# Kernel optimization log

Hardware: AMD Instinct MI355X
Metric: run time of the kernel (lower is better)

The kernel has to match this reference:

```python
import jax, jax.numpy as jnp
import numpy as np


def setup_inputs() -> dict:
    key = jax.random.key(0)
    ks = jax.random.split(key, 4)
    B, Tq, Tv = 8, 1024, 1024
    Dq, Dv, Do = 1024, 1024, 1024
    scale_q = 1.0 / np.sqrt(Dq)
    scale_2 = 1.0 / np.sqrt(Dq + Dv)
    return {
        "query": jax.random.normal(ks[0], (B, Tq, Dq), jnp.float32),
        "values": jax.random.normal(ks[1], (B, Tv, Dv), jnp.float32),
        "W1": jax.random.normal(ks[2], (Dv, Dq), jnp.float32) * scale_q,
        "b1": jnp.zeros((Dv,), jnp.float32),
        "W2": jax.random.normal(ks[3], (Do, Dq + Dv), jnp.float32) * scale_2,
        "b2": jnp.zeros((Do,), jnp.float32),
    }


def reference(query, values, W1, b1, W2, b2):
    # linear1: project query into values space  [B, Tq, Dv]
    q_resize = jnp.einsum("btd,vd->btv", query, W1) + b1
    # attention scores [B, Tq, Tv] and softmax over keys
    scores = jnp.einsum("bqd,bkd->bqk", q_resize, values)
    attn = jax.nn.softmax(scores, axis=-1)
    # attended values [B, Tq, Dv]
    attended = jnp.einsum("bqk,bkd->bqd", attn, values)
    # concat + linear2 + tanh
    feed = jnp.concatenate([attended, query], axis=-1)
    out = jnp.tanh(jnp.einsum("btf,of->bto", feed, W2) + b2)
    return out
```

## Files before the change

### kernel.cpp

```cpp
#include <hip/hip_runtime.h>
#include <hip/hip_bf16.h>

typedef __bf16 bf16x8 __attribute__((ext_vector_type(8)));
typedef float f32x4 __attribute__((ext_vector_type(4)));
typedef unsigned short u16;
typedef unsigned short us4 __attribute__((ext_vector_type(4)));
typedef unsigned int u32;

__device__ __forceinline__ u16 f2bf(float x) {
  union { float f; u32 u; } v; v.f = x;
  u32 r = v.u + 0x7FFFu + ((v.u >> 16) & 1u);
  return (u16)(r >> 16);
}
__device__ __forceinline__ float bf2f(u16 h) {
  union { u32 u; float f; } v; v.u = ((u32)h) << 16;
  return v.f;
}

__device__ __forceinline__ void glds16(const void* g, void* l) {
  __builtin_amdgcn_global_load_lds(
      (const __attribute__((address_space(1))) void*)g,
      (__attribute__((address_space(3))) void*)l, 16, 0, 0);
}

#define BARRIER_FENCED() do {                        \
  __builtin_amdgcn_sched_barrier(0);                 \
  __builtin_amdgcn_s_barrier();                      \
  __builtin_amdgcn_sched_barrier(0);                 \
} while (0)

template<int NSEG, int EPI>
__global__ __launch_bounds__(512, 2)
void gemm_bt(const u16* __restrict__ A, const u16* __restrict__ B,
             void* __restrict__ Cout, const float* __restrict__ bias,
             int K0, int lda, int ldb, int ldc,
             long sA, long sB, long sC, int nx, int ny)
{
  __shared__ __align__(1024) char lds_raw[3 * 49152];

  const int d = blockIdx.x;
  const int L = ((d & 7) << 5) | (d >> 3);
  const int nxy = nx * ny;
  const int bz = L / nxy;
  const int rr = L - bz * nxy;
  const int bx = rr / ny;
  const int by = rr - bx * ny;
  const int brow = bx * 256;
  const int bcol = by * 128;

  const int tid  = threadIdx.x;
  const int wid  = tid >> 6;
  const int lane = tid & 63;
  const int kh   = wid >> 2;
  const int wr   = (wid >> 1) & 1;
  const int wc   = wid & 1;

  const u16* Ab = A + (long)bz * sA + (long)brow * lda;
  const u16* Bb = B + (long)bz * sB + (long)bcol * ldb;

  f32x4 acc[8][4];
#pragma unroll
  for (int m = 0; m < 8; ++m)
#pragma unroll
    for (int n = 0; n < 4; ++n) acc[m][n] = (f32x4){0.f, 0.f, 0.f, 0.f};

  const int ksteps = (NSEG == 3) ? 16 : (K0 >> 6);
  const int NT = NSEG * ksteps;

  const int r15 = lane & 15;
  const int c16 = (lane >> 4) * 8;

  auto stage = [&](int t, int b) {
    int seg, kt;
    if (NSEG == 3) { seg = t >> 4; kt = (t & 15) << 6; }
    else           { seg = 0;      kt = t << 6; }
    const u16* Aseg = Ab + ((NSEG == 3 && seg == 1) ? K0 : 0) + kt;
    const u16* Bseg = Bb + ((NSEG == 3 && seg == 2) ? K0 : 0) + kt;
    u16* Lb = (u16*)(lds_raw + b * 49152);
#pragma unroll
    for (int q = 0; q < 4; ++q) {
      const int fa = wid * 4 + q;
      const int mi = fa >> 1, ki = fa & 1;
      glds16(Aseg + (long)(mi * 16 + r15) * lda + ki * 32 + c16, Lb + fa * 512);
    }
#pragma unroll
    for (int q = 0; q < 2; ++q) {
      const int fb = wid * 2 + q;
      const int nj = fb >> 1, ki = fb & 1;
      glds16(Bseg + (long)(nj * 16 + r15) * ldb + ki * 32 + c16,
             Lb + 16384 + fb * 512);
    }
  };

  stage(0, 0);
  stage(1, 1);
  asm volatile("s_waitcnt vmcnt(6)" ::: "memory");
  BARRIER_FENCED();

  int bufc = 0;
  for (int t = 0; t < NT; ++t) {
    const u16* Lb = (const u16*)(lds_raw + bufc * 49152);
    const u16* Af = Lb + (wr * 16 + kh) * 512 + lane * 8;
    const u16* Bf = Lb + 16384 + (wc * 8 + kh) * 512 + lane * 8;
    bf16x8 a[8], b[4];
#pragma unroll
    for (int m = 0; m < 8; ++m) a[m] = *(const bf16x8*)(Af + m * 1024);
#pragma unroll
    for (int n = 0; n < 4; ++n) b[n] = *(const bf16x8*)(Bf + n * 1024);

    if (t + 2 < NT) {
      int bufs = bufc + 2; if (bufs >= 3) bufs -= 3;
      stage(t + 2, bufs);
    }

    __builtin_amdgcn_s_setprio(1);
#pragma unroll
    for (int m = 0; m < 8; ++m)
#pragma unroll
      for (int n = 0; n < 4; ++n)
        acc[m][n] = __builtin_amdgcn_mfma_f32_16x16x32_bf16(a[m], b[n], acc[m][n], 0, 0, 0);
    __builtin_amdgcn_s_setprio(0);

    if (t + 2 < NT) { asm volatile("s_waitcnt vmcnt(6)" ::: "memory"); }
    else            { asm volatile("s_waitcnt vmcnt(0)" ::: "memory"); }
    BARRIER_FENCED();
    bufc = bufc + 1; if (bufc >= 3) bufc = 0;
  }

  float* red = (float*)lds_raw;
  const int p = wr * 2 + wc;
  if (kh == 1) {
#pragma unroll
    for (int m = 0; m < 8; ++m)
#pragma unroll
      for (int n = 0; n < 4; ++n)
        *(f32x4*)(red + ((p * 32 + m * 4 + n) * 64 + lane) * 4) = acc[m][n];
  }
  asm volatile("s_waitcnt lgkmcnt(0)" ::: "memory");
  BARRIER_FENCED();

  if (kh == 0) {
#pragma unroll
    for (int m = 0; m < 8; ++m)
#pragma unroll
      for (int n = 0; n < 4; ++n)
        acc[m][n] += *(const f32x4*)(red + ((p * 32 + m * 4 + n) * 64 + lane) * 4);

    const int crow0 = brow + wr * 128;
    const int ccol0 = bcol + wc * 64;
    const int orow  = (lane >> 4) * 4;
    const int ocol  = lane & 15;
#pragma unroll
    for (int m = 0; m < 8; ++m) {
#pragma unroll
      for (int n = 0; n < 4; ++n) {
        const int col = ccol0 + n * 16 + ocol;
        float bv = 0.f;
        if (EPI == 1 || EPI == 3) bv = bias[col];
#pragma unroll
        for (int j = 0; j < 4; ++j) {
          const int row = crow0 + m * 16 + orow + j;
          float v = acc[m][n][j] + bv;
          if (EPI == 0) {
            ((float*)Cout)[(long)bz * sC + (long)row * ldc + col] = v;
          } else if (EPI == 1) {
            u16 hi = f2bf(v);
            u16 lo = f2bf(v - bf2f(hi));
            u16* Co = (u16*)Cout + (long)bz * sC + (long)row * ldc;
            Co[col] = hi;
            Co[col + 1024] = lo;
          } else if (EPI == 2) {
            ((u16*)Cout)[(long)bz * sC + (long)row * ldc + col] = f2bf(v);
          } else {
            ((float*)Cout)[(long)bz * sC + (long)row * ldc + col] = tanhf(v);
          }
        }
      }
    }
  }
}

__global__ __launch_bounds__(256)
void split_pack(const float* __restrict__ X, u16* __restrict__ P,
                u16* __restrict__ FQ, long n4)
{
  long i = (long)blockIdx.x * 256 + threadIdx.x;
  const long stride = (long)gridDim.x * 256;
  for (; i < n4; i += stride) {
    float4 x = ((const float4*)X)[i];
    long e = i * 4;
    long row = e >> 10;
    int col = (int)(e & 1023);
    float xs[4] = {x.x, x.y, x.z, x.w};
    u16 h[4], l[4];
#pragma unroll
    for (int j = 0; j < 4; ++j) {
      h[j] = f2bf(xs[j]);
      l[j] = f2bf(xs[j] - bf2f(h[j]));
    }
    us4 hv = {h[0], h[1], h[2], h[3]};
    us4 lv = {l[0], l[1], l[2], l[3]};
    *(us4*)(P + row * 2048 + col) = hv;
    *(us4*)(P + row * 2048 + 1024 + col) = lv;
    if (FQ) *(us4*)(FQ + row * 2048 + 1024 + col) = hv;
  }
}

__global__ __launch_bounds__(256)
void conv_values(const float* __restrict__ V, u16* __restrict__ Vp,
                 u16* __restrict__ VT)
{
  __shared__ u16 tile[64][68];
  const int b  = blockIdx.z;
  const int d0 = blockIdx.x * 64;
  const int k0 = blockIdx.y * 64;
  const int t  = threadIdx.x;
  const int tr = t >> 4;
  const int tc = (t & 15) * 4;
  const float* Vb = V + (long)b * (1024L * 1024);
  u16* Vpb = Vp + (long)b * (1024L * 2048);
  u16* VTb = VT + (long)b * (1024L * 1024);

#pragma unroll
  for (int i = 0; i < 4; ++i) {
    int k = tr + i * 16;
    float4 x = *(const float4*)(Vb + (long)(k0 + k) * 1024 + d0 + tc);
    float xs[4] = {x.x, x.y, x.z, x.w};
    u16 h[4], l[4];
#pragma unroll
    for (int j = 0; j < 4; ++j) {
      h[j] = f2bf(xs[j]);
      l[j] = f2bf(xs[j] - bf2f(h[j]));
      tile[k][tc + j] = h[j];
    }
    us4 hv = {h[0], h[1], h[2], h[3]};
    us4 lv = {l[0], l[1], l[2], l[3]};
    *(us4*)(Vpb + (long)(k0 + k) * 2048 + d0 + tc) = hv;
    *(us4*)(Vpb + (long)(k0 + k) * 2048 + 1024 + d0 + tc) = lv;
  }
  __syncthreads();
#pragma unroll
  for (int i = 0; i < 4; ++i) {
    int d = tr + i * 16;
    int k = tc;
    us4 o = {tile[k][d], tile[k + 1][d], tile[k + 2][d], tile[k + 3][d]};
    *(us4*)(VTb + (long)(d0 + d) * 1024 + k0 + k) = o;
  }
}

__global__ __launch_bounds__(256)
void conv_cast(const float* __restrict__ X, u16* __restrict__ Y, long n4)
{
  long i = (long)blockIdx.x * 256 + threadIdx.x;
  const long stride = (long)gridDim.x * 256;
  for (; i < n4; i += stride) {
    float4 x = ((const float4*)X)[i];
    us4 o = {f2bf(x.x), f2bf(x.y), f2bf(x.z), f2bf(x.w)};
    *(us4*)(Y + i * 4) = o;
  }
}

__global__ __launch_bounds__(256)
void softmax_rows(const float* __restrict__ S, u16* __restrict__ A)
{
  const long row = blockIdx.x;
  const float* src = S + row * 1024;
  const int t = threadIdx.x;
  const int lane = t & 63, wid = t >> 6;
  float4 v = ((const float4*)src)[t];
  float m = fmaxf(fmaxf(v.x, v.y), fmaxf(v.z, v.w));
#pragma unroll
  for (int off = 32; off >= 1; off >>= 1)
    m = fmaxf(m, __shfl_xor(m, off));
  __shared__ float redm[4];
  if (lane == 0) redm[wid] = m;
  __syncthreads();
  m = fmaxf(fmaxf(redm[0], redm[1]), fmaxf(redm[2], redm[3]));
  float e0 = __expf(v.x - m), e1 = __expf(v.y - m);
  float e2 = __expf(v.z - m), e3 = __expf(v.w - m);
  float s = e0 + e1 + e2 + e3;
#pragma unroll
  for (int off = 32; off >= 1; off >>= 1)
    s += __shfl_xor(s, off);
  __shared__ float reds[4];
  if (lane == 0) reds[wid] = s;
  __syncthreads();
  s = reds[0] + reds[1] + reds[2] + reds[3];
  float inv = 1.0f / s;
  us4 o = {f2bf(e0 * inv), f2bf(e1 * inv), f2bf(e2 * inv), f2bf(e3 * inv)};
  ((us4*)(A + row * 1024))[t] = o;
}

extern "C" void kernel_launch(void* const* d_in, const int* in_sizes, int n_in,
                              void* d_out, int out_size, void* d_ws, size_t ws_size,
                              hipStream_t stream)
{
  const float* query  = (const float*)d_in[0];
  const float* values = (const float*)d_in[1];
  const float* W1     = (const float*)d_in[2];
  const float* b1     = (const float*)d_in[3];
  const float* W2     = (const float*)d_in[4];
  const float* b2     = (const float*)d_in[5];
  float* out = (float*)d_out;

  char* ws = (char*)d_ws;
  const long MB = 1024L * 1024;
  u16*   W1p    = (u16*)(ws);
  u16*   W2b    = (u16*)(ws + 4 * MB);
  u16*   Aq     = (u16*)(ws + 8 * MB);
  float* scores = (float*)(ws + 8 * MB);
  u16*   qr     = (u16*)(ws + 40 * MB);
  u16*   attn   = (u16*)(ws + 40 * MB);
  u16*   Vp     = (u16*)(ws + 72 * MB);
  u16*   VT     = (u16*)(ws + 104 * MB);
  u16*   feed   = (u16*)(ws + 120 * MB);

  split_pack<<<dim3(2048), dim3(256), 0, stream>>>(query, Aq, feed, (8192L * 1024) / 4);
  split_pack<<<dim3(1024), dim3(256), 0, stream>>>(W1, W1p, (u16*)nullptr, (1024L * 1024) / 4);
  conv_values<<<dim3(16, 16, 8), dim3(256), 0, stream>>>(values, Vp, VT);
  conv_cast<<<dim3(1024), dim3(256), 0, stream>>>(W2, W2b, (1024L * 2048) / 4);

  gemm_bt<3, 1><<<dim3(256), dim3(512), 0, stream>>>(
      Aq, W1p, qr, b1, 1024, 2048, 2048, 2048, 0L, 0L, 0L, 32, 8);

  gemm_bt<3, 0><<<dim3(256), dim3(512), 0, stream>>>(
      qr, Vp, scores, (const float*)nullptr, 1024, 2048, 2048, 1024,
      1024L * 2048, 1024L * 2048, 1024L * 1024, 4, 8);

  softmax_rows<<<dim3(8192), dim3(256), 0, stream>>>(scores, attn);

  gemm_bt<1, 2><<<dim3(256), dim3(512), 0, stream>>>(
      attn, VT, feed, (const float*)nullptr, 1024, 1024, 1024, 2048,
      1024L * 1024, 1024L * 1024, 1024L * 2048, 4, 8);

  gemm_bt<1, 3><<<dim3(256), dim3(512), 0, stream>>>(
      feed, W2b, out, b2, 2048, 2048, 2048, 1024, 0L, 0L, 0L, 32, 8);
}
```

Measured before the change: 395.2 us.

## Split GEMM k-step into four interleaved phases with barriers and staged loads

Breaks each k-step of the bf16 MFMA GEMM main loop into four phases. Each phase loads two A fragments from LDS, issues part of the next stage's global-to-LDS copies, and then runs eight MFMAs. Barriers and sched_barrier keep the waves in lockstep. The aim is to spread LDS reads and global loads across the MFMA work so they overlap better, in the style of ping-pong scheduling. The cost is many extra workgroup barriers per iteration, which can stall waves.

```diff
diff --git a/kernel.cpp b/kernel.cpp
--- a/kernel.cpp
+++ b/kernel.cpp
@@ -70,19 +70,22 @@
   const int r15 = lane & 15;
   const int c16 = (lane >> 4) * 8;
 
-  auto stage = [&](int t, int b) {
+  auto srcAB = [&](int t, const u16*& Aseg, const u16*& Bseg) {
     int seg, kt;
     if (NSEG == 3) { seg = t >> 4; kt = (t & 15) << 6; }
     else           { seg = 0;      kt = t << 6; }
-    const u16* Aseg = Ab + ((NSEG == 3 && seg == 1) ? K0 : 0) + kt;
-    const u16* Bseg = Bb + ((NSEG == 3 && seg == 2) ? K0 : 0) + kt;
-    u16* Lb = (u16*)(lds_raw + b * 49152);
-#pragma unroll
-    for (int q = 0; q < 4; ++q) {
+    Aseg = Ab + ((NSEG == 3 && seg == 1) ? K0 : 0) + kt;
+    Bseg = Bb + ((NSEG == 3 && seg == 2) ? K0 : 0) + kt;
+  };
+  auto stageA = [&](const u16* Aseg, u16* Lb, int q0) {
+#pragma unroll
+    for (int q = q0; q < q0 + 2; ++q) {
       const int fa = wid * 4 + q;
       const int mi = fa >> 1, ki = fa & 1;
       glds16(Aseg + (long)(mi * 16 + r15) * lda + ki * 32 + c16, Lb + fa * 512);
     }
+  };
+  auto stageB = [&](const u16* Bseg, u16* Lb) {
 #pragma unroll
     for (int q = 0; q < 2; ++q) {
       const int fb = wid * 2 + q;
@@ -92,8 +95,15 @@
     }
   };
 
-  stage(0, 0);
-  stage(1, 1);
+  {
+    const u16 *A0, *B0, *A1, *B1;
+    srcAB(0, A0, B0);
+    srcAB(1, A1, B1);
+    u16* L0 = (u16*)lds_raw;
+    u16* L1 = (u16*)(lds_raw + 49152);
+    stageA(A0, L0, 0); stageA(A0, L0, 2); stageB(B0, L0);
+    stageA(A1, L1, 0); stageA(A1, L1, 2); stageB(B1, L1);
+  }
   asm volatile("s_waitcnt vmcnt(6)" ::: "memory");
   BARRIER_FENCED();
 
@@ -102,28 +112,85 @@
     const u16* Lb = (const u16*)(lds_raw + bufc * 49152);
     const u16* Af = Lb + (wr * 16 + kh) * 512 + lane * 8;
     const u16* Bf = Lb + 16384 + (wc * 8 + kh) * 512 + lane * 8;
-    bf16x8 a[8], b[4];
-#pragma unroll
-    for (int m = 0; m < 8; ++m) a[m] = *(const bf16x8*)(Af + m * 1024);
-#pragma unroll
-    for (int n = 0; n < 4; ++n) b[n] = *(const bf16x8*)(Bf + n * 1024);
-
-    if (t + 2 < NT) {
+
+    const bool pre = (t + 2 < NT);
+    const u16 *Asg = nullptr, *Bsg = nullptr;
+    u16* Ls = nullptr;
+    if (pre) {
+      srcAB(t + 2, Asg, Bsg);
       int bufs = bufc + 2; if (bufs >= 3) bufs -= 3;
-      stage(t + 2, bufs);
-    }
-
-    __builtin_amdgcn_s_setprio(1);
-#pragma unroll
-    for (int m = 0; m < 8; ++m)
-#pragma unroll
-      for (int n = 0; n < 4; ++n)
-        acc[m][n] = __builtin_amdgcn_mfma_f32_16x16x32_bf16(a[m], b[n], acc[m][n], 0, 0, 0);
-    __builtin_amdgcn_s_setprio(0);
-
-    if (t + 2 < NT) { asm volatile("s_waitcnt vmcnt(6)" ::: "memory"); }
-    else            { asm volatile("s_waitcnt vmcnt(0)" ::: "memory"); }
-    BARRIER_FENCED();
+      Ls = (u16*)(lds_raw + bufs * 49152);
+    }
+
+    bf16x8 bfr[4];
+
+    {
+      bf16x8 a0 = *(const bf16x8*)(Af + 0 * 1024);
+      bf16x8 a1 = *(const bf16x8*)(Af + 1 * 1024);
+#pragma unroll
+      for (int n = 0; n < 4; ++n) bfr[n] = *(const bf16x8*)(Bf + n * 1024);
+      if (pre) stageA(Asg, Ls, 0);
+      BARRIER_FENCED();
+      asm volatile("s_waitcnt lgkmcnt(0)" ::: "memory");
+      __builtin_amdgcn_sched_barrier(0);
+      __builtin_amdgcn_s_setprio(1);
+#pragma unroll
+      for (int n = 0; n < 4; ++n) {
+        acc[0][n] = __builtin_amdgcn_mfma_f32_16x16x32_bf16(a0, bfr[n], acc[0][n], 0, 0, 0);
+        acc[1][n] = __builtin_amdgcn_mfma_f32_16x16x32_bf16(a1, bfr[n], acc[1][n], 0, 0, 0);
+      }
+      __builtin_amdgcn_s_setprio(0);
+      BARRIER_FENCED();
+    }
+    {
+      bf16x8 a2 = *(const bf16x8*)(Af + 2 * 1024);
+      bf16x8 a3 = *(const bf16x8*)(Af + 3 * 1024);
+      if (pre) stageA(Asg, Ls, 2);
+      BARRIER_FENCED();
+      asm volatile("s_waitcnt lgkmcnt(0)" ::: "memory");
+      __builtin_amdgcn_sched_barrier(0);
+      __builtin_amdgcn_s_setprio(1);
+#pragma unroll
+      for (int n = 0; n < 4; ++n) {
+        acc[2][n] = __builtin_amdgcn_mfma_f32_16x16x32_bf16(a2, bfr[n], acc[2][n], 0, 0, 0);
+        acc[3][n] = __builtin_amdgcn_mfma_f32_16x16x32_bf16(a3, bfr[n], acc[3][n], 0, 0, 0);
+      }
+      __builtin_amdgcn_s_setprio(0);
+      BARRIER_FENCED();
+    }
+    {
+      bf16x8 a4 = *(const bf16x8*)(Af + 4 * 1024);
+      bf16x8 a5 = *(const bf16x8*)(Af + 5 * 1024);
+      if (pre) stageB(Bsg, Ls);
+      BARRIER_FENCED();
+      asm volatile("s_waitcnt lgkmcnt(0)" ::: "memory");
+      __builtin_amdgcn_sched_barrier(0);
+      __builtin_amdgcn_s_setprio(1);
+#pragma unroll
+      for (int n = 0; n < 4; ++n) {
+        acc[4][n] = __builtin_amdgcn_mfma_f32_16x16x32_bf16(a4, bfr[n], acc[4][n], 0, 0, 0);
+        acc[5][n] = __builtin_amdgcn_mfma_f32_16x16x32_bf16(a5, bfr[n], acc[5][n], 0, 0, 0);
+      }
+      __builtin_amdgcn_s_setprio(0);
+      BARRIER_FENCED();
+    }
+    {
+      bf16x8 a6 = *(const bf16x8*)(Af + 6 * 1024);
+      bf16x8 a7 = *(const bf16x8*)(Af + 7 * 1024);
+      BARRIER_FENCED();
+      asm volatile("s_waitcnt lgkmcnt(0)" ::: "memory");
+      __builtin_amdgcn_sched_barrier(0);
+      __builtin_amdgcn_s_setprio(1);
+#pragma unroll
+      for (int n = 0; n < 4; ++n) {
+        acc[6][n] = __builtin_amdgcn_mfma_f32_16x16x32_bf16(a6, bfr[n], acc[6][n], 0, 0, 0);
+        acc[7][n] = __builtin_amdgcn_mfma_f32_16x16x32_bf16(a7, bfr[n], acc[7][n], 0, 0, 0);
+      }
+      __builtin_amdgcn_s_setprio(0);
+      if (pre) { asm volatile("s_waitcnt vmcnt(6)" ::: "memory"); }
+      else     { asm volatile("s_waitcnt vmcnt(0)" ::: "memory"); }
+      BARRIER_FENCED();
+    }
     bufc = bufc + 1; if (bufc >= 3) bufc = 0;
   }
 
```

Measured after the change: 398.5 us. About the same (+0.8%).

## Replace split-K wave pairs with 4x2 output-tiled waves and staged half-K loads

Applied to the files above, without the earlier changes.

The eight waves no longer split the K dimension in halves with an LDS reduction at the end. Each wave now owns a 64x64 output sub-tile over the full K range, so the end-of-kernel reduction goes away and accumulator registers halve. The per-step K=64 tile is processed in two halves, with global-to-LDS prefetch split across the halves and extra barriers. This can improve occupancy and interleave loads with MFMA, but the added barriers per step may cost synchronization overhead and wave-level reuse changes.

```diff
diff --git a/kernel.cpp b/kernel.cpp
--- a/kernel.cpp
+++ b/kernel.cpp
@@ -51,16 +51,15 @@
   const int tid  = threadIdx.x;
   const int wid  = tid >> 6;
   const int lane = tid & 63;
-  const int kh   = wid >> 2;
-  const int wr   = (wid >> 1) & 1;
+  const int wr   = wid >> 1;
   const int wc   = wid & 1;
 
   const u16* Ab = A + (long)bz * sA + (long)brow * lda;
   const u16* Bb = B + (long)bz * sB + (long)bcol * ldb;
 
-  f32x4 acc[8][4];
-#pragma unroll
-  for (int m = 0; m < 8; ++m)
+  f32x4 acc[4][4];
+#pragma unroll
+  for (int m = 0; m < 4; ++m)
 #pragma unroll
     for (int n = 0; n < 4; ++n) acc[m][n] = (f32x4){0.f, 0.f, 0.f, 0.f};
 
@@ -70,110 +69,125 @@
   const int r15 = lane & 15;
   const int c16 = (lane >> 4) * 8;
 
-  auto stage = [&](int t, int b) {
+  auto srcAB = [&](int t, const u16*& Aseg, const u16*& Bseg) {
     int seg, kt;
     if (NSEG == 3) { seg = t >> 4; kt = (t & 15) << 6; }
     else           { seg = 0;      kt = t << 6; }
-    const u16* Aseg = Ab + ((NSEG == 3 && seg == 1) ? K0 : 0) + kt;
-    const u16* Bseg = Bb + ((NSEG == 3 && seg == 2) ? K0 : 0) + kt;
-    u16* Lb = (u16*)(lds_raw + b * 49152);
-#pragma unroll
-    for (int q = 0; q < 4; ++q) {
+    Aseg = Ab + ((NSEG == 3 && seg == 1) ? K0 : 0) + kt;
+    Bseg = Bb + ((NSEG == 3 && seg == 2) ? K0 : 0) + kt;
+  };
+  auto stageA = [&](const u16* Aseg, u16* Lb, int q0) {
+#pragma unroll
+    for (int q = q0; q < q0 + 2; ++q) {
       const int fa = wid * 4 + q;
       const int mi = fa >> 1, ki = fa & 1;
       glds16(Aseg + (long)(mi * 16 + r15) * lda + ki * 32 + c16, Lb + fa * 512);
     }
-#pragma unroll
-    for (int q = 0; q < 2; ++q) {
-      const int fb = wid * 2 + q;
-      const int nj = fb >> 1, ki = fb & 1;
-      glds16(Bseg + (long)(nj * 16 + r15) * ldb + ki * 32 + c16,
-             Lb + 16384 + fb * 512);
-    }
   };
-
-  stage(0, 0);
-  stage(1, 1);
+  auto stageB = [&](const u16* Bseg, u16* Lb, int q) {
+    const int fb = wid * 2 + q;
+    const int nj = fb >> 1, ki = fb & 1;
+    glds16(Bseg + (long)(nj * 16 + r15) * ldb + ki * 32 + c16,
+           Lb + 16384 + fb * 512);
+  };
+
+  {
+    const u16 *A0, *B0, *A1, *B1;
+    srcAB(0, A0, B0);
+    srcAB(1, A1, B1);
+    u16* L0 = (u16*)lds_raw;
+    u16* L1 = (u16*)(lds_raw + 49152);
+    stageA(A0, L0, 0); stageA(A0, L0, 2); stageB(B0, L0, 0); stageB(B0, L0, 1);
+    stageA(A1, L1, 0); stageA(A1, L1, 2); stageB(B1, L1, 0); stageB(B1, L1, 1);
+  }
   asm volatile("s_waitcnt vmcnt(6)" ::: "memory");
   BARRIER_FENCED();
 
   int bufc = 0;
   for (int t = 0; t < NT; ++t) {
     const u16* Lb = (const u16*)(lds_raw + bufc * 49152);
-    const u16* Af = Lb + (wr * 16 + kh) * 512 + lane * 8;
-    const u16* Bf = Lb + 16384 + (wc * 8 + kh) * 512 + lane * 8;
-    bf16x8 a[8], b[4];
-#pragma unroll
-    for (int m = 0; m < 8; ++m) a[m] = *(const bf16x8*)(Af + m * 1024);
-#pragma unroll
-    for (int n = 0; n < 4; ++n) b[n] = *(const bf16x8*)(Bf + n * 1024);
-
-    if (t + 2 < NT) {
+    const u16* Af = Lb + (wr * 8) * 512 + lane * 8;
+    const u16* Bf = Lb + 16384 + (wc * 8) * 512 + lane * 8;
+
+    const bool pre = (t + 2 < NT);
+    const u16 *Asg = nullptr, *Bsg = nullptr;
+    u16* Ls = nullptr;
+    if (pre) {
+      srcAB(t + 2, Asg, Bsg);
       int bufs = bufc + 2; if (bufs >= 3) bufs -= 3;
-      stage(t + 2, bufs);
-    }
-
-    __builtin_amdgcn_s_setprio(1);
-#pragma unroll
-    for (int m = 0; m < 8; ++m)
-#pragma unroll
-      for (int n = 0; n < 4; ++n)
-        acc[m][n] = __builtin_amdgcn_mfma_f32_16x16x32_bf16(a[m], b[n], acc[m][n], 0, 0, 0);
-    __builtin_amdgcn_s_setprio(0);
-
-    if (t + 2 < NT) { asm volatile("s_waitcnt vmcnt(6)" ::: "memory"); }
-    else            { asm volatile("s_waitcnt vmcnt(0)" ::: "memory"); }
-    BARRIER_FENCED();
+      Ls = (u16*)(lds_raw + bufs * 49152);
+    }
+
+    {
+      bf16x8 a[4], b[4];
+#pragma unroll
+      for (int m = 0; m < 4; ++m) a[m] = *(const bf16x8*)(Af + (m * 2 + 0) * 512);
+#pragma unroll
+      for (int n = 0; n < 4; ++n) b[n] = *(const bf16x8*)(Bf + (n * 2 + 0) * 512);
+      if (pre) { stageA(Asg, Ls, 0); stageB(Bsg, Ls, 0); }
+      BARRIER_FENCED();
+      asm volatile("s_waitcnt lgkmcnt(0)" ::: "memory");
+      __builtin_amdgcn_sched_barrier(0);
+      __builtin_amdgcn_s_setprio(1);
+#pragma unroll
+      for (int m = 0; m < 4; ++m)
+#pragma unroll
+        for (int n = 0; n < 4; ++n)
+          acc[m][n] = __builtin_amdgcn_mfma_f32_16x16x32_bf16(a[m], b[n], acc[m][n], 0, 0, 0);
+      __builtin_amdgcn_s_setprio(0);
+      BARRIER_FENCED();
+    }
+    {
+      bf16x8 a[4], b[4];
+#pragma unroll
+      for (int m = 0; m < 4; ++m) a[m] = *(const bf16x8*)(Af + (m * 2 + 1) * 512);
+#pragma unroll
+      for (int n = 0; n < 4; ++n) b[n] = *(const bf16x8*)(Bf + (n * 2 + 1) * 512);
+      if (pre) { stageA(Asg, Ls, 2); stageB(Bsg, Ls, 1); }
+      BARRIER_FENCED();
+      asm volatile("s_waitcnt lgkmcnt(0)" ::: "memory");
+      __builtin_amdgcn_sched_barrier(0);
+      __builtin_amdgcn_s_setprio(1);
+#pragma unroll
+      for (int m = 0; m < 4; ++m)
+#pragma unroll
+        for (int n = 0; n < 4; ++n)
+          acc[m][n] = __builtin_amdgcn_mfma_f32_16x16x32_bf16(a[m], b[n], acc[m][n], 0, 0, 0);
+      __builtin_amdgcn_s_setprio(0);
+      if (pre) { asm volatile("s_waitcnt vmcnt(6)" ::: "memory"); }
+      else     { asm volatile("s_waitcnt vmcnt(0)" ::: "memory"); }
+      BARRIER_FENCED();
+    }
     bufc = bufc + 1; if (bufc >= 3) bufc = 0;
   }
 
-  float* red = (float*)lds_raw;
-  const int p = wr * 2 + wc;
-  if (kh == 1) {
-#pragma unroll
-    for (int m = 0; m < 8; ++m)
-#pragma unroll
-      for (int n = 0; n < 4; ++n)
-        *(f32x4*)(red + ((p * 32 + m * 4 + n) * 64 + lane) * 4) = acc[m][n];
-  }
-  asm volatile("s_waitcnt lgkmcnt(0)" ::: "memory");
-  BARRIER_FENCED();
-
-  if (kh == 0) {
-#pragma unroll
-    for (int m = 0; m < 8; ++m)
-#pragma unroll
-      for (int n = 0; n < 4; ++n)
-        acc[m][n] += *(const f32x4*)(red + ((p * 32 + m * 4 + n) * 64 + lane) * 4);
-
-    const int crow0 = brow + wr * 128;
-    const int ccol0 = bcol + wc * 64;
-    const int orow  = (lane >> 4) * 4;
-    const int ocol  = lane & 15;
-#pragma unroll
-    for (int m = 0; m < 8; ++m) {
-#pragma unroll
-      for (int n = 0; n < 4; ++n) {
-        const int col = ccol0 + n * 16 + ocol;
-        float bv = 0.f;
-        if (EPI == 1 || EPI == 3) bv = bias[col];
-#pragma unroll
-        for (int j = 0; j < 4; ++j) {
-          const int row = crow0 + m * 16 + orow + j;
-          float v = acc[m][n][j] + bv;
-          if (EPI == 0) {
-            ((float*)Cout)[(long)bz * sC + (long)row * ldc + col] = v;
-          } else if (EPI == 1) {
-            u16 hi = f2bf(v);
-            u16 lo = f2bf(v - bf2f(hi));
-            u16* Co = (u16*)Cout + (long)bz * sC + (long)row * ldc;
-            Co[col] = hi;
-            Co[col + 1024] = lo;
-          } else if (EPI == 2) {
-            ((u16*)Cout)[(long)bz * sC + (long)row * ldc + col] = f2bf(v);
-          } else {
-            ((float*)Cout)[(long)bz * sC + (long)row * ldc + col] = tanhf(v);
-          }
+  const int crow0 = brow + wr * 64;
+  const int ccol0 = bcol + wc * 64;
+  const int orow  = (lane >> 4) * 4;
+  const int ocol  = lane & 15;
+#pragma unroll
+  for (int m = 0; m < 4; ++m) {
+#pragma unroll
+    for (int n = 0; n < 4; ++n) {
+      const int col = ccol0 + n * 16 + ocol;
+      float bv = 0.f;
+      if (EPI == 1 || EPI == 3) bv = bias[col];
+#pragma unroll
+      for (int j = 0; j < 4; ++j) {
+        const int row = crow0 + m * 16 + orow + j;
+        float v = acc[m][n][j] + bv;
+        if (EPI == 0) {
+          ((float*)Cout)[(long)bz * sC + (long)row * ldc + col] = v;
+        } else if (EPI == 1) {
+          u16 hi = f2bf(v);
+          u16 lo = f2bf(v - bf2f(hi));
+          u16* Co = (u16*)Cout + (long)bz * sC + (long)row * ldc;
+          Co[col] = hi;
+          Co[col + 1024] = lo;
+        } else if (EPI == 2) {
+          ((u16*)Cout)[(long)bz * sC + (long)row * ldc + col] = f2bf(v);
+        } else {
+          ((float*)Cout)[(long)bz * sC + (long)row * ldc + col] = tanhf(v);
         }
       }
     }
```

Result: faster. 378.1 us (-4.4%).
